# Optimization experiments

Measured on AMD Instinct MI355X. Metric: run time of the kernel, lower is better.

The kernel has to match this reference:

```python
import jax, jax.numpy as jnp
import numpy as np

N = 100000
E = 1200000
D = 64
EPS = 0.1
GAMMA = 0.1


def gcn_conv(x, row, col, norm, phiW, n):
    # GCNConv(bias=False): xW then normalized sum aggregation (self-loops already in row/col)
    xw = x @ phiW.T                                   # [N, D]
    msg = xw[row] * norm[:, None]                     # [E+N, D] gather + scale
    return jax.ops.segment_sum(msg, col, num_segments=n)


def antisym_conv(x, row, col, norm, W, phiW, b):
    n, d = x.shape
    aW = W - W.T - GAMMA * jnp.eye(d, dtype=x.dtype)  # antisymmetric part minus gamma*I
    h = jnp.tanh(x @ aW.T + gcn_conv(x, row, col, norm, phiW, n) + b)
    return x + EPS * h                                # num_iters = 1


def _prep_edges(edge_index, n, dtype):
    # add self loops (fill weight 1.0) and compute symmetric GCN normalization
    loop = jnp.arange(n, dtype=edge_index.dtype)
    row = jnp.concatenate([edge_index[0], loop])
    col = jnp.concatenate([edge_index[1], loop])
    deg = jax.ops.segment_sum(jnp.ones(row.shape, dtype), col, num_segments=n)
    dinv = jnp.where(deg > 0, jax.lax.rsqrt(deg), 0.0)
    norm = dinv[row] * dinv[col]
    return row, col, norm


def setup_inputs() -> dict:
    key = jax.random.key(0)
    ks = jax.random.split(key, 10)
    s = 1.0 / np.sqrt(D)
    return {
        "x": jax.random.normal(ks[0], (N, D), jnp.float32),
        "W1": jax.random.uniform(ks[1], (D, D), jnp.float32, -s, s),
        "phiW1": jax.random.uniform(ks[2], (D, D), jnp.float32, -s, s),
        "b1": jax.random.uniform(ks[3], (D,), jnp.float32, -s, s),
        "W2": jax.random.uniform(ks[4], (D, D), jnp.float32, -s, s),
        "phiW2": jax.random.uniform(ks[5], (D, D), jnp.float32, -s, s),
        "b2": jax.random.uniform(ks[6], (D,), jnp.float32, -s, s),
        "outW": jax.random.uniform(ks[7], (1, D), jnp.float32, -s, s),
        "outb": jax.random.uniform(ks[8], (1,), jnp.float32, -s, s),
        "edge_index": jax.random.randint(ks[9], (2, E), 0, N, jnp.int64 if jax.config.jax_enable_x64 else jnp.int32),
    }


def reference(x, W1, phiW1, b1, W2, phiW2, b2, outW, outb, edge_index):
    row, col, norm = _prep_edges(edge_index, x.shape[0], x.dtype)
    x = jnp.maximum(antisym_conv(x, row, col, norm, W1, phiW1, b1), 0.0)
    x = jnp.maximum(antisym_conv(x, row, col, norm, W2, phiW2, b2), 0.0)
    return (x @ outW.T + outb)[:, 0]  # squeeze(-1)
```

## Files before the change

### kernel.cpp

```cpp
#include <hip/hip_runtime.h>
#include <math.h>

#define DD 64
#define NSLICE 8
#define NCHUNK 128
static constexpr float GAMMA_C = 0.1f;
static constexpr float EPS_C = 0.1f;

__global__ __launch_bounds__(256) void k_prep(const float* __restrict__ W1,
                                              const float* __restrict__ phiW1,
                                              const float* __restrict__ W2,
                                              const float* __restrict__ phiW2,
                                              float* __restrict__ aWT1,
                                              float* __restrict__ phiWT1,
                                              float* __restrict__ aWT2,
                                              float* __restrict__ phiWT2) {
  int idx = blockIdx.x * 256 + threadIdx.x;
  if (idx >= 4096) return;
  int k = idx >> 6, j = idx & 63;
  float g = (j == k) ? GAMMA_C : 0.f;
  aWT1[idx] = W1[j * 64 + k] - W1[k * 64 + j] - g;
  aWT2[idx] = W2[j * 64 + k] - W2[k * 64 + j] - g;
  phiWT1[idx] = phiW1[j * 64 + k];
  phiWT2[idx] = phiW2[j * 64 + k];
}

__global__ __launch_bounds__(256) void k_hist(const int* __restrict__ col,
                                              int* __restrict__ hist, int e, int n) {
  int slice = blockIdx.x & (NSLICE - 1);
  int chunk = blockIdx.x >> 3;
  int lo = (int)((long long)n * slice / NSLICE);
  int hi = (int)((long long)n * (slice + 1) / NSLICE);
  int per = (e + NCHUNK - 1) / NCHUNK;
  int s = chunk * per;
  int t = min(e, s + per);
  for (int i = s + threadIdx.x; i < t; i += 256) {
    int c = col[i];
    if (c >= lo && c < hi) atomicAdd(&hist[c], 1);
  }
}

__global__ __launch_bounds__(256) void k_scan1(const int* __restrict__ hist,
                                               int* __restrict__ rs,
                                               int* __restrict__ bsum, int n) {
  __shared__ int wtot[4];
  int b = blockIdx.x, t = threadIdx.x;
  int base = b * 2048 + t * 8;
  int v[8];
  int s = 0;
#pragma unroll
  for (int u = 0; u < 8; ++u) {
    int idx = base + u;
    v[u] = (idx < n) ? hist[idx] : 0;
    s += v[u];
  }
  int lane = t & 63, wid = t >> 6;
  int ws = s;
#pragma unroll
  for (int d = 1; d < 64; d <<= 1) {
    int o = __shfl_up(ws, d);
    if (lane >= d) ws += o;
  }
  if (lane == 63) wtot[wid] = ws;
  __syncthreads();
  int off = 0;
  for (int w = 0; w < wid; ++w) off += wtot[w];
  int run = ws - s + off;
#pragma unroll
  for (int u = 0; u < 8; ++u) {
    int idx = base + u;
    if (idx < n) rs[idx] = run;
    run += v[u];
  }
  if (t == 255) bsum[b] = run;
}

__global__ void k_scan2(const int* __restrict__ bsum, int* __restrict__ boff,
                        int nb, int* __restrict__ rs, int n, int e) {
  int t = threadIdx.x;
  int v = (t < nb) ? bsum[t] : 0;
  int s = v;
#pragma unroll
  for (int d = 1; d < 64; d <<= 1) {
    int o = __shfl_up(s, d);
    if (t >= d) s += o;
  }
  if (t < nb) boff[t] = s - v;
  if (t == 0) rs[n] = e;
}

__global__ __launch_bounds__(256) void k_scan3_dinv(int* __restrict__ rs,
                                                    const int* __restrict__ boff,
                                                    const int* __restrict__ hist,
                                                    float* __restrict__ dinv, int n) {
  int i = blockIdx.x * blockDim.x + threadIdx.x;
  if (i < n) {
    rs[i] += boff[i >> 11];
    dinv[i] = rsqrtf((float)(hist[i] + 1));
  }
}

__global__ __launch_bounds__(256) void k_fill(const int* __restrict__ row,
                                              const int* __restrict__ col,
                                              const int* __restrict__ rs,
                                              int* __restrict__ fillc,
                                              int* __restrict__ csr, int e, int n) {
  int slice = blockIdx.x & (NSLICE - 1);
  int chunk = blockIdx.x >> 3;
  int lo = (int)((long long)n * slice / NSLICE);
  int hi = (int)((long long)n * (slice + 1) / NSLICE);
  int per = (e + NCHUNK - 1) / NCHUNK;
  int s = chunk * per;
  int t = min(e, s + per);
  for (int i = s + threadIdx.x; i < t; i += 256) {
    int c = col[i];
    if (c >= lo && c < hi) {
      int p = atomicAdd(&fillc[c], 1);
      csr[rs[c] + p] = row[i];
    }
  }
}

__global__ __launch_bounds__(256, 4) void k_xw(const float* __restrict__ x,
                                               const float* __restrict__ phiWT,
                                               const float* __restrict__ dinv,
                                               unsigned short* __restrict__ xwh,
                                               int n) {
  int lane = threadIdx.x & 63;
  int gw = __builtin_amdgcn_readfirstlane(
      (int)((blockIdx.x * blockDim.x + threadIdx.x) >> 6));
  int nw = (gridDim.x * blockDim.x) >> 6;
  float w[64];
#pragma unroll
  for (int k = 0; k < 64; ++k) w[k] = phiWT[k * 64 + lane];
  for (int i = gw; i < n; i += nw) {
    const float* xr = x + (size_t)i * DD;
    float dv = dinv[i];
    float a0 = 0.f, a1 = 0.f, a2 = 0.f, a3 = 0.f;
#pragma unroll
    for (int k = 0; k < 64; k += 4) {
      a0 = fmaf(xr[k + 0], w[k + 0], a0);
      a1 = fmaf(xr[k + 1], w[k + 1], a1);
      a2 = fmaf(xr[k + 2], w[k + 2], a2);
      a3 = fmaf(xr[k + 3], w[k + 3], a3);
    }
    float r = dv * ((a0 + a1) + (a2 + a3));
    unsigned int u = __float_as_uint(r);
    unsigned int rb = (u + 0x7FFFu + ((u >> 16) & 1u)) >> 16;
    xwh[(size_t)i * DD + lane] = (unsigned short)rb;
  }
}

template <bool FINAL>
__global__ __launch_bounds__(256, 4) void k_agg(const float* __restrict__ xin,
                                                const unsigned short* __restrict__ xwh,
                                                const float* __restrict__ aWT,
                                                const float* __restrict__ b,
                                                const int* __restrict__ csr,
                                                const int* __restrict__ rs,
                                                const float* __restrict__ dinv,
                                                const float* __restrict__ outW,
                                                const float* __restrict__ outb,
                                                float* __restrict__ xo,
                                                float* __restrict__ out, int n) {
  int lane = threadIdx.x & 63;
  int gw = __builtin_amdgcn_readfirstlane(
      (int)((blockIdx.x * blockDim.x + threadIdx.x) >> 6));
  int nw = (gridDim.x * blockDim.x) >> 6;
  float w[64];
#pragma unroll
  for (int k = 0; k < 64; ++k) w[k] = aWT[k * 64 + lane];
  float bj = b[lane];
  float ow = FINAL ? outW[lane] : 0.f;
  for (int i = 2 * gw; i < n; i += 2 * nw) {
    bool hasB = (i + 1) < n;
    int s = rs[i];
    int mid = rs[i + 1];
    int t = hasB ? rs[i + 2] : mid;
    size_t oA = (size_t)i * DD + lane;
    size_t oB = oA + DD;
    float accA[4] = {__uint_as_float((unsigned int)xwh[oA] << 16), 0.f, 0.f, 0.f};
    float accB[4] = {hasB ? __uint_as_float((unsigned int)xwh[oB] << 16) : 0.f,
                     0.f, 0.f, 0.f};
    int k = s;
    for (; k + 7 < t; k += 8) {
      int r[8];
#pragma unroll
      for (int u = 0; u < 8; ++u) r[u] = csr[k + u];
      float v[8];
#pragma unroll
      for (int u = 0; u < 8; ++u)
        v[u] = __uint_as_float((unsigned int)xwh[(size_t)r[u] * DD + lane] << 16);
#pragma unroll
      for (int u = 0; u < 8; ++u) {
        float sA = (k + u < mid) ? 1.f : 0.f;
        accA[u & 3] = fmaf(v[u], sA, accA[u & 3]);
        accB[u & 3] = fmaf(v[u], 1.f - sA, accB[u & 3]);
      }
    }
    for (; k < t; ++k) {
      float v = __uint_as_float((unsigned int)xwh[(size_t)csr[k] * DD + lane] << 16);
      float sA = (k < mid) ? 1.f : 0.f;
      accA[0] = fmaf(v, sA, accA[0]);
      accB[0] = fmaf(v, 1.f - sA, accB[0]);
    }
    {
      float aggr = dinv[i] * ((accA[0] + accA[1]) + (accA[2] + accA[3]));
      const float* xr = xin + (size_t)i * DD;
      float l0 = 0.f, l1 = 0.f, l2 = 0.f, l3 = 0.f;
#pragma unroll
      for (int kk = 0; kk < 64; kk += 4) {
        l0 = fmaf(xr[kk + 0], w[kk + 0], l0);
        l1 = fmaf(xr[kk + 1], w[kk + 1], l1);
        l2 = fmaf(xr[kk + 2], w[kk + 2], l2);
        l3 = fmaf(xr[kk + 3], w[kk + 3], l3);
      }
      float tot = ((l0 + l1) + (l2 + l3)) + bj + aggr;
      float val = fmaxf(fmaf(EPS_C, tanhf(tot), xin[oA]), 0.f);
      if (FINAL) {
        float p = val * ow;
#pragma unroll
        for (int sg = 32; sg > 0; sg >>= 1) p += __shfl_xor(p, sg);
        if (lane == 0) out[i] = p + outb[0];
      } else {
        xo[oA] = val;
      }
    }
    if (hasB) {
      float aggr = dinv[i + 1] * ((accB[0] + accB[1]) + (accB[2] + accB[3]));
      const float* xr = xin + (size_t)(i + 1) * DD;
      float l0 = 0.f, l1 = 0.f, l2 = 0.f, l3 = 0.f;
#pragma unroll
      for (int kk = 0; kk < 64; kk += 4) {
        l0 = fmaf(xr[kk + 0], w[kk + 0], l0);
        l1 = fmaf(xr[kk + 1], w[kk + 1], l1);
        l2 = fmaf(xr[kk + 2], w[kk + 2], l2);
        l3 = fmaf(xr[kk + 3], w[kk + 3], l3);
      }
      float tot = ((l0 + l1) + (l2 + l3)) + bj + aggr;
      float val = fmaxf(fmaf(EPS_C, tanhf(tot), xin[oB]), 0.f);
      if (FINAL) {
        float p = val * ow;
#pragma unroll
        for (int sg = 32; sg > 0; sg >>= 1) p += __shfl_xor(p, sg);
        if (lane == 0) out[i + 1] = p + outb[0];
      } else {
        xo[oB] = val;
      }
    }
  }
}

extern "C" void kernel_launch(void* const* d_in, const int* in_sizes, int n_in,
                              void* d_out, int out_size, void* d_ws, size_t ws_size,
                              hipStream_t stream) {
  const float* x     = (const float*)d_in[0];
  const float* W1    = (const float*)d_in[1];
  const float* phiW1 = (const float*)d_in[2];
  const float* b1    = (const float*)d_in[3];
  const float* W2    = (const float*)d_in[4];
  const float* phiW2 = (const float*)d_in[5];
  const float* b2    = (const float*)d_in[6];
  const float* outW  = (const float*)d_in[7];
  const float* outb  = (const float*)d_in[8];
  const int*   ei    = (const int*)d_in[9];

  int n = in_sizes[0] / DD;
  int e = in_sizes[9] / 2;
  const int* row = ei;
  const int* col = ei + e;
  float* out = (float*)d_out;

  char* w = (char*)d_ws;
  auto carve = [&](size_t bytes) {
    char* p = w;
    w += (bytes + 255) & ~(size_t)255;
    return p;
  };
  float* aWT1   = (float*)carve(4096 * 4);
  float* phiWT1 = (float*)carve(4096 * 4);
  float* aWT2   = (float*)carve(4096 * 4);
  float* phiWT2 = (float*)carve(4096 * 4);
  int*   hist   = (int*)carve((size_t)n * 4);
  int*   fillc  = (int*)carve((size_t)n * 4);
  int*   rs     = (int*)carve(((size_t)n + 1) * 4);
  int*   bsum   = (int*)carve(64 * 4);
  int*   boff   = (int*)carve(64 * 4);
  float* dinv   = (float*)carve((size_t)n * 4);
  int*   csr    = (int*)carve((size_t)e * 4);
  unsigned short* xwh = (unsigned short*)carve((size_t)n * DD * 2);
  float* x1     = (float*)carve((size_t)n * DD * 4);

  int nb_n   = (n + 255) / 256;
  int nb_sl  = NSLICE * NCHUNK;
  int nb_sc1 = (n + 2047) / 2048;
  int nb_xw  = 1024;
  int nb_ag  = 2048;

  size_t zbytes = (size_t)((char*)fillc - (char*)hist) + (size_t)n * 4;
  hipMemsetAsync(hist, 0, zbytes, stream);

  k_prep<<<16, 256, 0, stream>>>(W1, phiW1, W2, phiW2, aWT1, phiWT1, aWT2, phiWT2);
  k_hist<<<nb_sl, 256, 0, stream>>>(col, hist, e, n);
  k_scan1<<<nb_sc1, 256, 0, stream>>>(hist, rs, bsum, n);
  k_scan2<<<1, 64, 0, stream>>>(bsum, boff, nb_sc1, rs, n, e);
  k_scan3_dinv<<<nb_n, 256, 0, stream>>>(rs, boff, hist, dinv, n);
  k_fill<<<nb_sl, 256, 0, stream>>>(row, col, rs, fillc, csr, e, n);

  k_xw<<<nb_xw, 256, 0, stream>>>(x, phiWT1, dinv, xwh, n);
  k_agg<false><<<nb_ag, 256, 0, stream>>>(x, xwh, aWT1, b1, csr, rs, dinv,
                                          nullptr, nullptr, x1, nullptr, n);

  k_xw<<<nb_xw, 256, 0, stream>>>(x1, phiWT2, dinv, xwh, n);
  k_agg<true><<<nb_ag, 256, 0, stream>>>(x1, xwh, aWT2, b2, csr, rs, dinv,
                                         outW, outb, nullptr, out, n);
}
```

Measured before the change: 492.7 us.

## Process four nodes per wave with shared-memory weights and double-buffered gathers

Both the xW and aggregation kernels now hold the 64x64 weight matrix in LDS instead of 64 registers per lane. Each wave handles four consecutive nodes per iteration. The aggregation gathers the merged edge range in double-buffered batches of eight and splits it into per-node sums with cumulative masked accumulators. This is meant to cut register pressure, raise memory-level parallelism in the gather, and amortise weight loads across four rows. In exchange it adds LDS reads and extra masking arithmetic, and it changes the floating-point summation order by differencing the cumulative sums.

```diff
diff --git a/kernel.cpp b/kernel.cpp
--- a/kernel.cpp
+++ b/kernel.cpp
@@ -6,6 +6,10 @@
 #define NCHUNK 128
 static constexpr float GAMMA_C = 0.1f;
 static constexpr float EPS_C = 0.1f;
+
+__device__ __forceinline__ float bf16u(unsigned short h) {
+  return __uint_as_float((unsigned int)h << 16);
+}
 
 __global__ __launch_bounds__(256) void k_prep(const float* __restrict__ W1,
                                               const float* __restrict__ phiW1,
@@ -126,28 +130,45 @@
                                                const float* __restrict__ dinv,
                                                unsigned short* __restrict__ xwh,
                                                int n) {
+  __shared__ float lw[4096];
+  for (int u = threadIdx.x; u < 4096; u += 256) lw[u] = phiWT[u];
+  __syncthreads();
   int lane = threadIdx.x & 63;
   int gw = __builtin_amdgcn_readfirstlane(
       (int)((blockIdx.x * blockDim.x + threadIdx.x) >> 6));
   int nw = (gridDim.x * blockDim.x) >> 6;
-  float w[64];
-#pragma unroll
-  for (int k = 0; k < 64; ++k) w[k] = phiWT[k * 64 + lane];
-  for (int i = gw; i < n; i += nw) {
-    const float* xr = x + (size_t)i * DD;
-    float dv = dinv[i];
-    float a0 = 0.f, a1 = 0.f, a2 = 0.f, a3 = 0.f;
-#pragma unroll
-    for (int k = 0; k < 64; k += 4) {
-      a0 = fmaf(xr[k + 0], w[k + 0], a0);
-      a1 = fmaf(xr[k + 1], w[k + 1], a1);
-      a2 = fmaf(xr[k + 2], w[k + 2], a2);
-      a3 = fmaf(xr[k + 3], w[k + 3], a3);
-    }
-    float r = dv * ((a0 + a1) + (a2 + a3));
-    unsigned int u = __float_as_uint(r);
-    unsigned int rb = (u + 0x7FFFu + ((u >> 16) & 1u)) >> 16;
-    xwh[(size_t)i * DD + lane] = (unsigned short)rb;
+  for (int i = 4 * gw; i < n; i += 4 * nw) {
+    int j1 = min(i + 1, n - 1), j2 = min(i + 2, n - 1), j3 = min(i + 3, n - 1);
+    const float* xr0 = x + (size_t)i * DD;
+    const float* xr1 = x + (size_t)j1 * DD;
+    const float* xr2 = x + (size_t)j2 * DD;
+    const float* xr3 = x + (size_t)j3 * DD;
+    float l0 = 0.f, l1 = 0.f, l2 = 0.f, l3 = 0.f;
+#pragma unroll
+    for (int blk = 0; blk < 8; ++blk) {
+      float w8[8];
+#pragma unroll
+      for (int u = 0; u < 8; ++u) w8[u] = lw[(blk * 8 + u) * 64 + lane];
+#pragma unroll
+      for (int u = 0; u < 8; ++u) {
+        int kk = blk * 8 + u;
+        l0 = fmaf(xr0[kk], w8[u], l0);
+        l1 = fmaf(xr1[kk], w8[u], l1);
+        l2 = fmaf(xr2[kk], w8[u], l2);
+        l3 = fmaf(xr3[kk], w8[u], l3);
+      }
+    }
+    float r0 = dinv[i] * l0, r1 = dinv[j1] * l1;
+    float r2 = dinv[j2] * l2, r3 = dinv[j3] * l3;
+    auto pack = [](float r) {
+      unsigned int u = __float_as_uint(r);
+      return (unsigned short)((u + 0x7FFFu + ((u >> 16) & 1u)) >> 16);
+    };
+    size_t o = (size_t)i * DD + lane;
+    xwh[o] = pack(r0);
+    if (i + 1 < n) xwh[o + DD] = pack(r1);
+    if (i + 2 < n) xwh[o + 2 * DD] = pack(r2);
+    if (i + 3 < n) xwh[o + 3 * DD] = pack(r3);
   }
 }
 
@@ -163,90 +184,118 @@
                                                 const float* __restrict__ outb,
                                                 float* __restrict__ xo,
                                                 float* __restrict__ out, int n) {
+  __shared__ float lw[4096];
+  for (int u = threadIdx.x; u < 4096; u += 256) lw[u] = aWT[u];
+  __syncthreads();
   int lane = threadIdx.x & 63;
   int gw = __builtin_amdgcn_readfirstlane(
       (int)((blockIdx.x * blockDim.x + threadIdx.x) >> 6));
   int nw = (gridDim.x * blockDim.x) >> 6;
-  float w[64];
-#pragma unroll
-  for (int k = 0; k < 64; ++k) w[k] = aWT[k * 64 + lane];
   float bj = b[lane];
   float ow = FINAL ? outW[lane] : 0.f;
-  for (int i = 2 * gw; i < n; i += 2 * nw) {
-    bool hasB = (i + 1) < n;
-    int s = rs[i];
-    int mid = rs[i + 1];
-    int t = hasB ? rs[i + 2] : mid;
-    size_t oA = (size_t)i * DD + lane;
-    size_t oB = oA + DD;
-    float accA[4] = {__uint_as_float((unsigned int)xwh[oA] << 16), 0.f, 0.f, 0.f};
-    float accB[4] = {hasB ? __uint_as_float((unsigned int)xwh[oB] << 16) : 0.f,
-                     0.f, 0.f, 0.f};
-    int k = s;
-    for (; k + 7 < t; k += 8) {
-      int r[8];
-#pragma unroll
-      for (int u = 0; u < 8; ++u) r[u] = csr[k + u];
-      float v[8];
-#pragma unroll
-      for (int u = 0; u < 8; ++u)
-        v[u] = __uint_as_float((unsigned int)xwh[(size_t)r[u] * DD + lane] << 16);
+  for (int i = 4 * gw; i < n; i += 4 * nw) {
+    int i1 = min(i + 1, n), i2 = min(i + 2, n), i3 = min(i + 3, n), i4 = min(i + 4, n);
+    int e0 = rs[i], m1 = rs[i1], m2 = rs[i2], m3 = rs[i3], e4 = rs[i4];
+    float t0 = 0.f, t1 = 0.f, t2 = 0.f, t3 = 0.f;
+    if (e0 < e4) {
+      int e4m1 = e4 - 1;
+      int rA[8], rB[8];
+      float vA[8], vB[8];
+      auto loadB = [&](int kb, int* rX, float* vX) {
+#pragma unroll
+        for (int u = 0; u < 8; ++u) rX[u] = csr[min(kb + u, e4m1)];
+#pragma unroll
+        for (int u = 0; u < 8; ++u)
+          vX[u] = bf16u(xwh[(size_t)rX[u] * DD + lane]);
+      };
+      auto consB = [&](int kb, const float* vX) {
+#pragma unroll
+        for (int u = 0; u < 8; ++u) {
+          int ke = kb + u;
+          float vv = (ke < e4) ? vX[u] : 0.f;
+          t0 += vv;
+          t1 = fmaf((ke >= m1) ? 1.f : 0.f, vv, t1);
+          t2 = fmaf((ke >= m2) ? 1.f : 0.f, vv, t2);
+          t3 = fmaf((ke >= m3) ? 1.f : 0.f, vv, t3);
+        }
+      };
+      int k = e0;
+      loadB(k, rA, vA);
+      while (true) {
+        int kn = k + 8;
+        if (kn < e4) {
+          loadB(kn, rB, vB);
+          consB(k, vA);
+        } else {
+          consB(k, vA);
+          break;
+        }
+        k = kn;
+        kn = k + 8;
+        if (kn < e4) {
+          loadB(kn, rA, vA);
+          consB(k, vB);
+        } else {
+          consB(k, vB);
+          break;
+        }
+        k = kn;
+      }
+    }
+    size_t o0 = (size_t)i * DD + lane;
+    float s0 = bf16u(xwh[o0]);
+    float s1 = (i + 1 < n) ? bf16u(xwh[o0 + DD]) : 0.f;
+    float s2 = (i + 2 < n) ? bf16u(xwh[o0 + 2 * DD]) : 0.f;
+    float s3 = (i + 3 < n) ? bf16u(xwh[o0 + 3 * DD]) : 0.f;
+    float g0 = dinv[i] * ((t0 - t1) + s0);
+    float g1 = (i + 1 < n) ? dinv[i1] * ((t1 - t2) + s1) : 0.f;
+    float g2 = (i + 2 < n) ? dinv[i2] * ((t2 - t3) + s2) : 0.f;
+    float g3 = (i + 3 < n) ? dinv[i3] * (t3 + s3) : 0.f;
+    int j1 = min(i + 1, n - 1), j2 = min(i + 2, n - 1), j3 = min(i + 3, n - 1);
+    const float* xr0 = xin + (size_t)i * DD;
+    const float* xr1 = xin + (size_t)j1 * DD;
+    const float* xr2 = xin + (size_t)j2 * DD;
+    const float* xr3 = xin + (size_t)j3 * DD;
+    float l0 = 0.f, l1 = 0.f, l2 = 0.f, l3 = 0.f;
+#pragma unroll
+    for (int blk = 0; blk < 8; ++blk) {
+      float w8[8];
+#pragma unroll
+      for (int u = 0; u < 8; ++u) w8[u] = lw[(blk * 8 + u) * 64 + lane];
 #pragma unroll
       for (int u = 0; u < 8; ++u) {
-        float sA = (k + u < mid) ? 1.f : 0.f;
-        accA[u & 3] = fmaf(v[u], sA, accA[u & 3]);
-        accB[u & 3] = fmaf(v[u], 1.f - sA, accB[u & 3]);
-      }
-    }
-    for (; k < t; ++k) {
-      float v = __uint_as_float((unsigned int)xwh[(size_t)csr[k] * DD + lane] << 16);
-      float sA = (k < mid) ? 1.f : 0.f;
-      accA[0] = fmaf(v, sA, accA[0]);
-      accB[0] = fmaf(v, 1.f - sA, accB[0]);
-    }
-    {
-      float aggr = dinv[i] * ((accA[0] + accA[1]) + (accA[2] + accA[3]));
-      const float* xr = xin + (size_t)i * DD;
-      float l0 = 0.f, l1 = 0.f, l2 = 0.f, l3 = 0.f;
-#pragma unroll
-      for (int kk = 0; kk < 64; kk += 4) {
-        l0 = fmaf(xr[kk + 0], w[kk + 0], l0);
-        l1 = fmaf(xr[kk + 1], w[kk + 1], l1);
-        l2 = fmaf(xr[kk + 2], w[kk + 2], l2);
-        l3 = fmaf(xr[kk + 3], w[kk + 3], l3);
-      }
-      float tot = ((l0 + l1) + (l2 + l3)) + bj + aggr;
-      float val = fmaxf(fmaf(EPS_C, tanhf(tot), xin[oA]), 0.f);
-      if (FINAL) {
-        float p = val * ow;
-#pragma unroll
-        for (int sg = 32; sg > 0; sg >>= 1) p += __shfl_xor(p, sg);
-        if (lane == 0) out[i] = p + outb[0];
-      } else {
-        xo[oA] = val;
-      }
-    }
-    if (hasB) {
-      float aggr = dinv[i + 1] * ((accB[0] + accB[1]) + (accB[2] + accB[3]));
-      const float* xr = xin + (size_t)(i + 1) * DD;
-      float l0 = 0.f, l1 = 0.f, l2 = 0.f, l3 = 0.f;
-#pragma unroll
-      for (int kk = 0; kk < 64; kk += 4) {
-        l0 = fmaf(xr[kk + 0], w[kk + 0], l0);
-        l1 = fmaf(xr[kk + 1], w[kk + 1], l1);
-        l2 = fmaf(xr[kk + 2], w[kk + 2], l2);
-        l3 = fmaf(xr[kk + 3], w[kk + 3], l3);
-      }
-      float tot = ((l0 + l1) + (l2 + l3)) + bj + aggr;
-      float val = fmaxf(fmaf(EPS_C, tanhf(tot), xin[oB]), 0.f);
-      if (FINAL) {
-        float p = val * ow;
-#pragma unroll
-        for (int sg = 32; sg > 0; sg >>= 1) p += __shfl_xor(p, sg);
-        if (lane == 0) out[i + 1] = p + outb[0];
-      } else {
-        xo[oB] = val;
-      }
+        int kk = blk * 8 + u;
+        l0 = fmaf(xr0[kk], w8[u], l0);
+        l1 = fmaf(xr1[kk], w8[u], l1);
+        l2 = fmaf(xr2[kk], w8[u], l2);
+        l3 = fmaf(xr3[kk], w8[u], l3);
+      }
+    }
+    float val0 = fmaxf(fmaf(EPS_C, tanhf(l0 + bj + g0), xin[o0]), 0.f);
+    float val1 = fmaxf(fmaf(EPS_C, tanhf(l1 + bj + g1), xin[(size_t)j1 * DD + lane]), 0.f);
+    float val2 = fmaxf(fmaf(EPS_C, tanhf(l2 + bj + g2), xin[(size_t)j2 * DD + lane]), 0.f);
+    float val3 = fmaxf(fmaf(EPS_C, tanhf(l3 + bj + g3), xin[(size_t)j3 * DD + lane]), 0.f);
+    if (FINAL) {
+      float p0 = val0 * ow, p1 = val1 * ow, p2 = val2 * ow, p3 = val3 * ow;
+#pragma unroll
+      for (int sg = 32; sg > 0; sg >>= 1) {
+        p0 += __shfl_xor(p0, sg);
+        p1 += __shfl_xor(p1, sg);
+        p2 += __shfl_xor(p2, sg);
+        p3 += __shfl_xor(p3, sg);
+      }
+      if (lane == 0) {
+        float ob = outb[0];
+        out[i] = p0 + ob;
+        if (i + 1 < n) out[i + 1] = p1 + ob;
+        if (i + 2 < n) out[i + 2] = p2 + ob;
+        if (i + 3 < n) out[i + 3] = p3 + ob;
+      }
+    } else {
+      xo[o0] = val0;
+      if (i + 1 < n) xo[o0 + DD] = val1;
+      if (i + 2 < n) xo[o0 + 2 * DD] = val2;
+      if (i + 3 < n) xo[o0 + 3 * DD] = val3;
     }
   }
 }
```

New measurement: 474.4 us. 1.04x faster.

## Aggregate edges per node tile with LDS atomics and packed CSR entries

Applied to the files above, without the earlier changes.

The aggregation kernel now gives each block a tile of 128 destination nodes. Its four waves split the tile's edge range evenly and accumulate gathered bf16 features into a shared-memory buffer with atomic adds, which spreads work evenly across high-degree nodes instead of assigning two nodes per wave. The local destination index is packed into the top 8 bits of each CSR entry, so it limits source indices to 24 bits. The xW kernel also processes four rows per wave to reuse weight registers, at the cost of LDS atomic contention and 32KB of shared memory per block, which lowers occupancy.

```diff
diff --git a/kernel.cpp b/kernel.cpp
--- a/kernel.cpp
+++ b/kernel.cpp
@@ -2,10 +2,15 @@
 #include <math.h>
 
 #define DD 64
+#define TILE 128
 #define NSLICE 8
 #define NCHUNK 128
 static constexpr float GAMMA_C = 0.1f;
 static constexpr float EPS_C = 0.1f;
+
+__device__ __forceinline__ float bf16u(unsigned short h) {
+  return __uint_as_float((unsigned int)h << 16);
+}
 
 __global__ __launch_bounds__(256) void k_prep(const float* __restrict__ W1,
                                               const float* __restrict__ phiW1,
@@ -104,7 +109,8 @@
                                               const int* __restrict__ col,
                                               const int* __restrict__ rs,
                                               int* __restrict__ fillc,
-                                              int* __restrict__ csr, int e, int n) {
+                                              unsigned int* __restrict__ csr,
+                                              int e, int n) {
   int slice = blockIdx.x & (NSLICE - 1);
   int chunk = blockIdx.x >> 3;
   int lo = (int)((long long)n * slice / NSLICE);
@@ -116,7 +122,7 @@
     int c = col[i];
     if (c >= lo && c < hi) {
       int p = atomicAdd(&fillc[c], 1);
-      csr[rs[c] + p] = row[i];
+      csr[rs[c] + p] = ((unsigned int)(c & (TILE - 1)) << 24) | (unsigned int)row[i];
     }
   }
 }
@@ -133,120 +139,108 @@
   float w[64];
 #pragma unroll
   for (int k = 0; k < 64; ++k) w[k] = phiWT[k * 64 + lane];
-  for (int i = gw; i < n; i += nw) {
-    const float* xr = x + (size_t)i * DD;
-    float dv = dinv[i];
-    float a0 = 0.f, a1 = 0.f, a2 = 0.f, a3 = 0.f;
-#pragma unroll
-    for (int k = 0; k < 64; k += 4) {
-      a0 = fmaf(xr[k + 0], w[k + 0], a0);
-      a1 = fmaf(xr[k + 1], w[k + 1], a1);
-      a2 = fmaf(xr[k + 2], w[k + 2], a2);
-      a3 = fmaf(xr[k + 3], w[k + 3], a3);
+  for (int i = 4 * gw; i < n; i += 4 * nw) {
+    int j1 = min(i + 1, n - 1), j2 = min(i + 2, n - 1), j3 = min(i + 3, n - 1);
+    const float* xr0 = x + (size_t)i * DD;
+    const float* xr1 = x + (size_t)j1 * DD;
+    const float* xr2 = x + (size_t)j2 * DD;
+    const float* xr3 = x + (size_t)j3 * DD;
+    float l0 = 0.f, l1 = 0.f, l2 = 0.f, l3 = 0.f;
+#pragma unroll
+    for (int kk = 0; kk < 64; ++kk) {
+      l0 = fmaf(xr0[kk], w[kk], l0);
+      l1 = fmaf(xr1[kk], w[kk], l1);
+      l2 = fmaf(xr2[kk], w[kk], l2);
+      l3 = fmaf(xr3[kk], w[kk], l3);
     }
-    float r = dv * ((a0 + a1) + (a2 + a3));
-    unsigned int u = __float_as_uint(r);
-    unsigned int rb = (u + 0x7FFFu + ((u >> 16) & 1u)) >> 16;
-    xwh[(size_t)i * DD + lane] = (unsigned short)rb;
+    float r0 = dinv[i] * l0, r1 = dinv[j1] * l1;
+    float r2 = dinv[j2] * l2, r3 = dinv[j3] * l3;
+    auto pack = [](float r) {
+      unsigned int u = __float_as_uint(r);
+      return (unsigned short)((u + 0x7FFFu + ((u >> 16) & 1u)) >> 16);
+    };
+    size_t o = (size_t)i * DD + lane;
+    xwh[o] = pack(r0);
+    if (i + 1 < n) xwh[o + DD] = pack(r1);
+    if (i + 2 < n) xwh[o + 2 * DD] = pack(r2);
+    if (i + 3 < n) xwh[o + 3 * DD] = pack(r3);
   }
 }
 
 template <bool FINAL>
-__global__ __launch_bounds__(256, 4) void k_agg(const float* __restrict__ xin,
+__global__ __launch_bounds__(256, 3) void k_agg(const float* __restrict__ xin,
                                                 const unsigned short* __restrict__ xwh,
                                                 const float* __restrict__ aWT,
                                                 const float* __restrict__ b,
-                                                const int* __restrict__ csr,
+                                                const unsigned int* __restrict__ csr,
                                                 const int* __restrict__ rs,
                                                 const float* __restrict__ dinv,
                                                 const float* __restrict__ outW,
                                                 const float* __restrict__ outb,
                                                 float* __restrict__ xo,
                                                 float* __restrict__ out, int n) {
-  int lane = threadIdx.x & 63;
-  int gw = __builtin_amdgcn_readfirstlane(
-      (int)((blockIdx.x * blockDim.x + threadIdx.x) >> 6));
-  int nw = (gridDim.x * blockDim.x) >> 6;
+  __shared__ float lacc[TILE * DD];
+  int tid = threadIdx.x;
+  int lane = tid & 63;
+  int wv = tid >> 6;
+  int tLo = blockIdx.x * TILE;
+  int tHi = min(tLo + TILE, n);
   float w[64];
 #pragma unroll
   for (int k = 0; k < 64; ++k) w[k] = aWT[k * 64 + lane];
   float bj = b[lane];
   float ow = FINAL ? outW[lane] : 0.f;
-  for (int i = 2 * gw; i < n; i += 2 * nw) {
-    bool hasB = (i + 1) < n;
-    int s = rs[i];
-    int mid = rs[i + 1];
-    int t = hasB ? rs[i + 2] : mid;
-    size_t oA = (size_t)i * DD + lane;
-    size_t oB = oA + DD;
-    float accA[4] = {__uint_as_float((unsigned int)xwh[oA] << 16), 0.f, 0.f, 0.f};
-    float accB[4] = {hasB ? __uint_as_float((unsigned int)xwh[oB] << 16) : 0.f,
-                     0.f, 0.f, 0.f};
-    int k = s;
-    for (; k + 7 < t; k += 8) {
-      int r[8];
-#pragma unroll
-      for (int u = 0; u < 8; ++u) r[u] = csr[k + u];
-      float v[8];
-#pragma unroll
-      for (int u = 0; u < 8; ++u)
-        v[u] = __uint_as_float((unsigned int)xwh[(size_t)r[u] * DD + lane] << 16);
-#pragma unroll
-      for (int u = 0; u < 8; ++u) {
-        float sA = (k + u < mid) ? 1.f : 0.f;
-        accA[u & 3] = fmaf(v[u], sA, accA[u & 3]);
-        accB[u & 3] = fmaf(v[u], 1.f - sA, accB[u & 3]);
-      }
+  for (int u = tid; u < TILE * DD; u += 256) lacc[u] = 0.f;
+  __syncthreads();
+  int eLo = rs[tLo];
+  int eHi = rs[tHi];
+  int cnt = eHi - eLo;
+  int per = (cnt + 3) >> 2;
+  int kLo = eLo + wv * per;
+  int kHi = min(eHi, kLo + per);
+  int k = kLo;
+  for (; k + 8 <= kHi; k += 8) {
+    unsigned int p[8];
+#pragma unroll
+    for (int u = 0; u < 8; ++u) p[u] = csr[k + u];
+    float v[8];
+#pragma unroll
+    for (int u = 0; u < 8; ++u)
+      v[u] = bf16u(xwh[(size_t)(p[u] & 0xFFFFFFu) * DD + lane]);
+#pragma unroll
+    for (int u = 0; u < 8; ++u)
+      atomicAdd(&lacc[(p[u] >> 24) * DD + lane], v[u]);
+  }
+  for (; k < kHi; ++k) {
+    unsigned int p = csr[k];
+    float v = bf16u(xwh[(size_t)(p & 0xFFFFFFu) * DD + lane]);
+    atomicAdd(&lacc[(p >> 24) * DD + lane], v);
+  }
+  __syncthreads();
+  int dlEnd = tHi - tLo;
+  int dlStop = min(wv * 32 + 32, dlEnd);
+  for (int dl = wv * 32; dl < dlStop; ++dl) {
+    int i = tLo + dl;
+    size_t o = (size_t)i * DD + lane;
+    float aggr = dinv[i] * (lacc[dl * DD + lane] + bf16u(xwh[o]));
+    const float* xr = xin + (size_t)i * DD;
+    float l0 = 0.f, l1 = 0.f, l2 = 0.f, l3 = 0.f;
+#pragma unroll
+    for (int kk = 0; kk < 64; kk += 4) {
+      l0 = fmaf(xr[kk + 0], w[kk + 0], l0);
+      l1 = fmaf(xr[kk + 1], w[kk + 1], l1);
+      l2 = fmaf(xr[kk + 2], w[kk + 2], l2);
+      l3 = fmaf(xr[kk + 3], w[kk + 3], l3);
     }
-    for (; k < t; ++k) {
-      float v = __uint_as_float((unsigned int)xwh[(size_t)csr[k] * DD + lane] << 16);
-      float sA = (k < mid) ? 1.f : 0.f;
-      accA[0] = fmaf(v, sA, accA[0]);
-      accB[0] = fmaf(v, 1.f - sA, accB[0]);
-    }
-    {
-      float aggr = dinv[i] * ((accA[0] + accA[1]) + (accA[2] + accA[3]));
-      const float* xr = xin + (size_t)i * DD;
-      float l0 = 0.f, l1 = 0.f, l2 = 0.f, l3 = 0.f;
-#pragma unroll
-      for (int kk = 0; kk < 64; kk += 4) {
-        l0 = fmaf(xr[kk + 0], w[kk + 0], l0);
-        l1 = fmaf(xr[kk + 1], w[kk + 1], l1);
-        l2 = fmaf(xr[kk + 2], w[kk + 2], l2);
-        l3 = fmaf(xr[kk + 3], w[kk + 3], l3);
-      }
-      float tot = ((l0 + l1) + (l2 + l3)) + bj + aggr;
-      float val = fmaxf(fmaf(EPS_C, tanhf(tot), xin[oA]), 0.f);
-      if (FINAL) {
-        float p = val * ow;
-#pragma unroll
-        for (int sg = 32; sg > 0; sg >>= 1) p += __shfl_xor(p, sg);
-        if (lane == 0) out[i] = p + outb[0];
-      } else {
-        xo[oA] = val;
-      }
-    }
-    if (hasB) {
-      float aggr = dinv[i + 1] * ((accB[0] + accB[1]) + (accB[2] + accB[3]));
-      const float* xr = xin + (size_t)(i + 1) * DD;
-      float l0 = 0.f, l1 = 0.f, l2 = 0.f, l3 = 0.f;
-#pragma unroll
-      for (int kk = 0; kk < 64; kk += 4) {
-        l0 = fmaf(xr[kk + 0], w[kk + 0], l0);
-        l1 = fmaf(xr[kk + 1], w[kk + 1], l1);
-        l2 = fmaf(xr[kk + 2], w[kk + 2], l2);
-        l3 = fmaf(xr[kk + 3], w[kk + 3], l3);
-      }
-      float tot = ((l0 + l1) + (l2 + l3)) + bj + aggr;
-      float val = fmaxf(fmaf(EPS_C, tanhf(tot), xin[oB]), 0.f);
-      if (FINAL) {
-        float p = val * ow;
-#pragma unroll
-        for (int sg = 32; sg > 0; sg >>= 1) p += __shfl_xor(p, sg);
-        if (lane == 0) out[i + 1] = p + outb[0];
-      } else {
-        xo[oB] = val;
-      }
+    float tot = ((l0 + l1) + (l2 + l3)) + bj + aggr;
+    float val = fmaxf(fmaf(EPS_C, tanhf(tot), xin[o]), 0.f);
+    if (FINAL) {
+      float p = val * ow;
+#pragma unroll
+      for (int sg = 32; sg > 0; sg >>= 1) p += __shfl_xor(p, sg);
+      if (lane == 0) out[i] = p + outb[0];
+    } else {
+      xo[o] = val;
     }
   }
 }
@@ -287,7 +281,7 @@
   int*   bsum   = (int*)carve(64 * 4);
   int*   boff   = (int*)carve(64 * 4);
   float* dinv   = (float*)carve((size_t)n * 4);
-  int*   csr    = (int*)carve((size_t)e * 4);
+  unsigned int* csr = (unsigned int*)carve((size_t)e * 4);
   unsigned short* xwh = (unsigned short*)carve((size_t)n * DD * 2);
   float* x1     = (float*)carve((size_t)n * DD * 4);
 
@@ -295,7 +289,7 @@
   int nb_sl  = NSLICE * NCHUNK;
   int nb_sc1 = (n + 2047) / 2048;
   int nb_xw  = 1024;
-  int nb_ag  = 2048;
+  int nb_ag  = (n + TILE - 1) / TILE;
 
   size_t zbytes = (size_t)((char*)fillc - (char*)hist) + (size_t)n * 4;
   hipMemsetAsync(hist, 0, zbytes, stream);
```

New measurement: 1.428 ms. 190% more time.
